# Kernel tuning notes

Measured on AMD Instinct MI355X. Metric: run time of the kernel, lower is better.

Reference implementation:

```python
import jax, jax.numpy as jnp
import numpy as np

N_HEAD = 12
D_HEAD = 64  # key_dim // n_head = 768 // 12


def sparsemax(z):
    # Martins & Astudillo (2016): projection of each row of z onto the simplex.
    K = z.shape[-1]
    z_sorted = -jnp.sort(-z, axis=-1)                      # descending sort
    cs = jnp.cumsum(z_sorted, axis=-1)
    r = jnp.arange(1, K + 1, dtype=z.dtype)
    support = (1.0 + r * z_sorted) > cs                    # support set indicator
    ksz = jnp.sum(support, axis=-1, keepdims=True)         # support size k(z)
    cs_k = jnp.take_along_axis(cs, ksz.astype(jnp.int32) - 1, axis=-1)
    tau = (cs_k - 1.0) / ksz.astype(z.dtype)               # threshold
    return jnp.maximum(z - tau, 0.0)


def setup_inputs() -> dict:
    key = jax.random.key(0)
    kq, kk, kv, kwq, kbq, kwk, kbk = jax.random.split(key, 7)
    B, L, D = 8, 1024, 768
    scale = 0.02
    return {
        "q": jax.random.normal(kq, (B, L, D), jnp.float32),
        "k": jax.random.normal(kk, (B, L, D), jnp.float32),
        "v": jax.random.normal(kv, (B, L, D), jnp.float32),
        "Wq": jax.random.normal(kwq, (D, D), jnp.float32) * scale,  # torch Linear weight [out,in]
        "bq": jax.random.normal(kbq, (D,), jnp.float32) * scale,
        "Wk": jax.random.normal(kwk, (D, D), jnp.float32) * scale,
        "bk": jax.random.normal(kbk, (D,), jnp.float32) * scale,
    }


def reference(q, k, v, Wq, bq, Wk, bk):
    B, Lq, _ = q.shape
    Lkv = k.shape[1]
    # project and split heads: [B, H, L, d_head]
    qh = (q @ Wq.T + bq).reshape(B, Lq, N_HEAD, D_HEAD).transpose(0, 2, 1, 3)
    kh = (k @ Wk.T + bk).reshape(B, Lkv, N_HEAD, D_HEAD).transpose(0, 2, 1, 3)
    inv_sqrt_d = jnp.asarray(1.0 / np.sqrt(D_HEAD), q.dtype)
    scores = jnp.einsum("bhqd,bhkd->bhqk", qh, kh) * inv_sqrt_d  # [B,H,Lq,Lkv]
    attn = sparsemax(scores)
    attn = attn.mean(axis=1)                                      # head-mean -> [B,Lq,Lkv]
    # eval mode: smooth_max is identity (training-only smoothing)
    output = jnp.einsum("bqk,bkd->bqd", attn, v)                  # [B,Lq,Dv]
    return output, attn
```

## Files before the change

kernel.cpp:

```cpp
#include <hip/hip_runtime.h>

#define BSZ 8
#define NH 12
#define LSEQ 1024
#define DMODEL 768
#define DHEAD 64
#define OUT_ELEMS 6291456
#define ATTN_ELEMS 8388608

typedef __attribute__((ext_vector_type(8))) short short8;
typedef __attribute__((ext_vector_type(4))) float f32x4;

__device__ __forceinline__ int   f2i(float x) { union { float f; int i; } c; c.f = x; return c.i; }
__device__ __forceinline__ float i2f(int x)   { union { int i; float f; } c; c.i = x; return c.f; }

__device__ __forceinline__ unsigned short f2bf(float x) {
    union { float f; unsigned u; } c; c.f = x;
    unsigned r = (c.u + 0x7FFF + ((c.u >> 16) & 1)) >> 16;
    return (unsigned short)r;
}
__device__ __forceinline__ float bf2f(unsigned short h) {
    union { float f; unsigned u; } c; c.u = ((unsigned)h) << 16;
    return c.f;
}
__device__ __forceinline__ void split2(float x, unsigned short& h, unsigned short& l) {
    h = f2bf(x);
    l = f2bf(x - bf2f(h));
}

template<int CTRL>
__device__ __forceinline__ float dppadd(float v) {
    return v + i2f(__builtin_amdgcn_update_dpp(0, f2i(v), CTRL, 0xF, 0xF, true));
}
template<int CTRL>
__device__ __forceinline__ float dppmax(float v) {
    return fmaxf(v, i2f(__builtin_amdgcn_update_dpp(f2i(v), f2i(v), CTRL, 0xF, 0xF, false)));
}

__device__ __forceinline__ void wsum2(float s[2]) {
#define WS(CTRL) _Pragma("unroll") for (int rr = 0; rr < 2; ++rr) { s[rr] = dppadd<CTRL>(s[rr]); }
    WS(0x111) WS(0x112) WS(0x114) WS(0x118) WS(0x142) WS(0x143)
#undef WS
#pragma unroll
    for (int rr = 0; rr < 2; ++rr) s[rr] = i2f(__builtin_amdgcn_readlane(f2i(s[rr]), 63));
}

__device__ __forceinline__ void wsummax2(float s[2], float m[2]) {
#define WS(CTRL) _Pragma("unroll") for (int rr = 0; rr < 2; ++rr) { s[rr] = dppadd<CTRL>(s[rr]); m[rr] = dppmax<CTRL>(m[rr]); }
    WS(0x111) WS(0x112) WS(0x114) WS(0x118) WS(0x142) WS(0x143)
#undef WS
#pragma unroll
    for (int rr = 0; rr < 2; ++rr) {
        s[rr] = i2f(__builtin_amdgcn_readlane(f2i(s[rr]), 63));
        m[rr] = i2f(__builtin_amdgcn_readlane(f2i(m[rr]), 63));
    }
}

__global__ __launch_bounds__(256) void proj_mfma(
    const float* __restrict__ qin, const float* __restrict__ kin,
    const float* __restrict__ Wq, const float* __restrict__ bq,
    const float* __restrict__ Wk, const float* __restrict__ bk,
    unsigned short* __restrict__ ws) {
    const float* A; const float* W; const float* bias;
    unsigned short* hi; unsigned short* lo;
    if (blockIdx.z == 0) { A = qin; W = Wq; bias = bq; hi = ws;                lo = ws + OUT_ELEMS; }
    else                 { A = kin; W = Wk; bias = bk; hi = ws + 2*OUT_ELEMS; lo = ws + 3*OUT_ELEMS; }

    __shared__ unsigned short Ah[128][32], Al[128][32];
    __shared__ unsigned short Bh[128][32], Bl[128][32];

    const int t    = threadIdx.x;
    const int lane = t & 63;
    const int w    = t >> 6;
    const int wr   = w >> 1, wc = w & 1;
    const int mrow = lane & 15, quad = lane >> 4;
    const int m0   = blockIdx.y * 128;
    const int n0   = blockIdx.x * 128;

    const int srow = t >> 3;
    const int scol = (t & 7) * 4;

    f32x4 acc[4][4];
#pragma unroll
    for (int i = 0; i < 4; ++i)
#pragma unroll
        for (int j = 0; j < 4; ++j) acc[i][j] = (f32x4){0.f, 0.f, 0.f, 0.f};

    for (int k0 = 0; k0 < DMODEL; k0 += 32) {
        float4 av[4], wv[4];
#pragma unroll
        for (int i = 0; i < 4; ++i) {
            av[i] = *(const float4*)&A[(size_t)(m0 + srow + i * 32) * DMODEL + k0 + scol];
            wv[i] = *(const float4*)&W[(size_t)(n0 + srow + i * 32) * DMODEL + k0 + scol];
        }
        __syncthreads();
#pragma unroll
        for (int i = 0; i < 4; ++i) {
            ushort4 h4, l4;
            split2(av[i].x, h4.x, l4.x); split2(av[i].y, h4.y, l4.y);
            split2(av[i].z, h4.z, l4.z); split2(av[i].w, h4.w, l4.w);
            *(ushort4*)&Ah[srow + i * 32][scol] = h4;
            *(ushort4*)&Al[srow + i * 32][scol] = l4;
            split2(wv[i].x, h4.x, l4.x); split2(wv[i].y, h4.y, l4.y);
            split2(wv[i].z, h4.z, l4.z); split2(wv[i].w, h4.w, l4.w);
            *(ushort4*)&Bh[srow + i * 32][scol] = h4;
            *(ushort4*)&Bl[srow + i * 32][scol] = l4;
        }
        __syncthreads();

        short8 ah[4], al[4], bh[4], bl[4];
#pragma unroll
        for (int i = 0; i < 4; ++i) {
            ah[i] = *(const short8*)&Ah[wr * 64 + i * 16 + mrow][quad * 8];
            al[i] = *(const short8*)&Al[wr * 64 + i * 16 + mrow][quad * 8];
            bh[i] = *(const short8*)&Bh[wc * 64 + i * 16 + mrow][quad * 8];
            bl[i] = *(const short8*)&Bl[wc * 64 + i * 16 + mrow][quad * 8];
        }
#pragma unroll
        for (int i = 0; i < 4; ++i)
#pragma unroll
            for (int j = 0; j < 4; ++j) {
                acc[i][j] = __builtin_amdgcn_mfma_f32_16x16x32_bf16(al[i], bh[j], acc[i][j], 0, 0, 0);
                acc[i][j] = __builtin_amdgcn_mfma_f32_16x16x32_bf16(ah[i], bl[j], acc[i][j], 0, 0, 0);
                acc[i][j] = __builtin_amdgcn_mfma_f32_16x16x32_bf16(ah[i], bh[j], acc[i][j], 0, 0, 0);
            }
    }

#pragma unroll
    for (int j = 0; j < 4; ++j) {
        const int ng = n0 + wc * 64 + j * 16 + mrow;
        const float bj = bias[ng];
        const int hh = ng >> 6, dd = ng & 63;
#pragma unroll
        for (int i = 0; i < 4; ++i) {
#pragma unroll
            for (int reg = 0; reg < 4; ++reg) {
                const int mg = m0 + wr * 64 + i * 16 + quad * 4 + reg;
                const float c = acc[i][j][reg] + bj;
                unsigned short ch, cl;
                split2(c, ch, cl);
                const size_t idx = (((size_t)(mg >> 10) * NH + hh) * LSEQ + (mg & 1023)) * DHEAD + dd;
                hi[idx] = ch;
                lo[idx] = cl;
            }
        }
    }
}

__global__ __launch_bounds__(512, 4) void attn_kernel(
    const unsigned short* __restrict__ ws, float* __restrict__ attn_out) {
    __shared__ float S[16 * 1024];

    const unsigned short* Qhi = ws;
    const unsigned short* Qlo = ws + OUT_ELEMS;
    const unsigned short* Khi = ws + 2 * OUT_ELEMS;
    const unsigned short* Klo = ws + 3 * OUT_ELEMS;

    const int t = threadIdx.x;
    const int lane = t & 63;
    const int w = t >> 6;
    const int b = blockIdx.y;
    const int q0 = blockIdx.x * 16;

    const int mrow = lane & 15;
    const int quad = lane >> 4;

    float macc[2][16];
#pragma unroll
    for (int rr = 0; rr < 2; ++rr)
#pragma unroll
        for (int j = 0; j < 16; ++j) macc[rr][j] = 0.f;

    for (int h = 0; h < NH; ++h) {
        const size_t hb = ((size_t)b * NH + h) * (LSEQ * DHEAD);

        const size_t aoff = hb + (size_t)(q0 + mrow) * DHEAD + quad * 8;
        short8 ah0 = *(const short8*)(Qhi + aoff);
        short8 ah1 = *(const short8*)(Qhi + aoff + 32);
        short8 al0 = *(const short8*)(Qlo + aoff);
        short8 al1 = *(const short8*)(Qlo + aoff + 32);

        __syncthreads();

#pragma unroll 2
        for (int nt = 0; nt < 8; ++nt) {
            const int n0 = w * 128 + nt * 16;
            const size_t boff = hb + (size_t)(n0 + mrow) * DHEAD + quad * 8;
            short8 bh0 = *(const short8*)(Khi + boff);
            short8 bh1 = *(const short8*)(Khi + boff + 32);
            short8 bl0 = *(const short8*)(Klo + boff);
            short8 bl1 = *(const short8*)(Klo + boff + 32);
            f32x4 d = {0.f, 0.f, 0.f, 0.f};
            d = __builtin_amdgcn_mfma_f32_16x16x32_bf16(al0, bh0, d, 0, 0, 0);
            d = __builtin_amdgcn_mfma_f32_16x16x32_bf16(ah0, bl0, d, 0, 0, 0);
            d = __builtin_amdgcn_mfma_f32_16x16x32_bf16(ah0, bh0, d, 0, 0, 0);
            d = __builtin_amdgcn_mfma_f32_16x16x32_bf16(al1, bh1, d, 0, 0, 0);
            d = __builtin_amdgcn_mfma_f32_16x16x32_bf16(ah1, bl1, d, 0, 0, 0);
            d = __builtin_amdgcn_mfma_f32_16x16x32_bf16(ah1, bh1, d, 0, 0, 0);
            const int swcol = (n0 + mrow) ^ (quad << 4);
#pragma unroll
            for (int reg = 0; reg < 4; ++reg)
                S[(quad * 4 + reg) * 1024 + swcol] = d[reg] * 0.125f;
        }
        __syncthreads();

        float z[2][16];
        float sv[2], mv[2];
#pragma unroll
        for (int rr = 0; rr < 2; ++rr) {
            const int r = w * 2 + rr;
            const int swz = (r >> 2) << 4;
#pragma unroll
            for (int c = 0; c < 4; ++c)
                *(f32x4*)&z[rr][c * 4] = *(const f32x4*)&S[r * 1024 + ((c * 256 + lane * 4) ^ swz)];
            float s0 = 0.f, s1 = 0.f, s2 = 0.f, s3 = 0.f;
            float m0 = z[rr][0], m1 = z[rr][1], m2 = z[rr][2], m3 = z[rr][3];
#pragma unroll
            for (int j = 0; j < 16; j += 4) {
                s0 += z[rr][j]; s1 += z[rr][j + 1]; s2 += z[rr][j + 2]; s3 += z[rr][j + 3];
            }
#pragma unroll
            for (int j = 4; j < 16; j += 4) {
                m0 = fmaxf(m0, z[rr][j]);     m1 = fmaxf(m1, z[rr][j + 1]);
                m2 = fmaxf(m2, z[rr][j + 2]); m3 = fmaxf(m3, z[rr][j + 3]);
            }
            sv[rr] = (s0 + s1) + (s2 + s3);
            mv[rr] = fmaxf(fmaxf(m0, m1), fmaxf(m2, m3));
        }
        wsummax2(sv, mv);

        float tau[2]; int prev[2]; bool done[2];
#pragma unroll
        for (int rr = 0; rr < 2; ++rr) {
            tau[rr] = fmaxf((sv[rr] - 1.0f) * (1.0f / 1024.0f), mv[rr] - 1.0f);
            prev[rr] = -1; done[rr] = false;
        }

        for (int it = 0; it < 64; ++it) {
            float sI[2]; int cI[2];
#pragma unroll
            for (int rr = 0; rr < 2; ++rr) {
                float a0 = 0.f, a1 = 0.f, a2 = 0.f, a3 = 0.f;
                int c = 0;
#pragma unroll
                for (int j = 0; j < 16; j += 4) {
                    bool g0 = z[rr][j]     > tau[rr];
                    bool g1 = z[rr][j + 1] > tau[rr];
                    bool g2 = z[rr][j + 2] > tau[rr];
                    bool g3 = z[rr][j + 3] > tau[rr];
                    c += __popcll(__ballot(g0)) + __popcll(__ballot(g1))
                       + __popcll(__ballot(g2)) + __popcll(__ballot(g3));
                    a0 += g0 ? z[rr][j]     : 0.f;
                    a1 += g1 ? z[rr][j + 1] : 0.f;
                    a2 += g2 ? z[rr][j + 2] : 0.f;
                    a3 += g3 ? z[rr][j + 3] : 0.f;
                }
                sI[rr] = (a0 + a1) + (a2 + a3);
                cI[rr] = c;
            }
            wsum2(sI);
            bool alldone = true;
#pragma unroll
            for (int rr = 0; rr < 2; ++rr) {
                if (!done[rr]) {
                    if (cI[rr] == prev[rr]) done[rr] = true;
                    else { tau[rr] = (sI[rr] - 1.0f) / (float)cI[rr]; prev[rr] = cI[rr]; }
                }
                alldone = alldone && done[rr];
            }
            if (alldone) break;
        }

#pragma unroll
        for (int rr = 0; rr < 2; ++rr)
#pragma unroll
            for (int j = 0; j < 16; ++j)
                macc[rr][j] += fmaxf(z[rr][j] - tau[rr], 0.f);
    }

    float* ao = attn_out + ((size_t)b * LSEQ + q0) * LSEQ;
#pragma unroll
    for (int rr = 0; rr < 2; ++rr) {
        const int r = w * 2 + rr;
#pragma unroll
        for (int c = 0; c < 4; ++c) {
            f32x4 o;
#pragma unroll
            for (int j = 0; j < 4; ++j) o[j] = macc[rr][c * 4 + j] * (1.0f / 12.0f);
            *(f32x4*)&ao[(size_t)r * LSEQ + c * 256 + lane * 4] = o;
        }
    }
}

__global__ __launch_bounds__(256) void out_mfma(
    const float* __restrict__ attn, const float* __restrict__ v,
    float* __restrict__ out) {
    const int b = blockIdx.z;
    const float* Ab = attn + (size_t)b * LSEQ * LSEQ;
    const float* Vb = v    + (size_t)b * LSEQ * DMODEL;
    float* Cb       = out  + (size_t)b * LSEQ * DMODEL;

    __shared__ unsigned short Ah[128][32], Al[128][32];
    __shared__ unsigned short Bh[128][36], Bl[128][36];

    const int t    = threadIdx.x;
    const int lane = t & 63;
    const int w    = t >> 6;
    const int wr   = w >> 1, wc = w & 1;
    const int mrow = lane & 15, quad = lane >> 4;
    const int m0   = blockIdx.y * 128;
    const int n0   = blockIdx.x * 128;

    const int srow = t >> 3;
    const int scol = (t & 7) * 4;
    const int bn   = t & 127;
    const int bk0  = (t >> 7) * 16;

    f32x4 acc[4][4];
#pragma unroll
    for (int i = 0; i < 4; ++i)
#pragma unroll
        for (int j = 0; j < 4; ++j) acc[i][j] = (f32x4){0.f, 0.f, 0.f, 0.f};

    for (int k0 = 0; k0 < LSEQ; k0 += 32) {
        float4 av[4];
#pragma unroll
        for (int i = 0; i < 4; ++i)
            av[i] = *(const float4*)&Ab[(size_t)(m0 + srow + i * 32) * LSEQ + k0 + scol];
        float bv[16];
#pragma unroll
        for (int i = 0; i < 16; ++i)
            bv[i] = Vb[(size_t)(k0 + bk0 + i) * DMODEL + n0 + bn];

        __syncthreads();
#pragma unroll
        for (int i = 0; i < 4; ++i) {
            ushort4 h4, l4;
            split2(av[i].x, h4.x, l4.x); split2(av[i].y, h4.y, l4.y);
            split2(av[i].z, h4.z, l4.z); split2(av[i].w, h4.w, l4.w);
            *(ushort4*)&Ah[srow + i * 32][scol] = h4;
            *(ushort4*)&Al[srow + i * 32][scol] = l4;
        }
#pragma unroll
        for (int g = 0; g < 4; ++g) {
            ushort4 h4, l4;
            split2(bv[g * 4 + 0], h4.x, l4.x); split2(bv[g * 4 + 1], h4.y, l4.y);
            split2(bv[g * 4 + 2], h4.z, l4.z); split2(bv[g * 4 + 3], h4.w, l4.w);
            *(ushort4*)&Bh[bn][bk0 + g * 4] = h4;
            *(ushort4*)&Bl[bn][bk0 + g * 4] = l4;
        }
        __syncthreads();

        short8 ah[4], al[4], bh[4], bl[4];
#pragma unroll
        for (int i = 0; i < 4; ++i) {
            ah[i] = *(const short8*)&Ah[wr * 64 + i * 16 + mrow][quad * 8];
            al[i] = *(const short8*)&Al[wr * 64 + i * 16 + mrow][quad * 8];
        }
#pragma unroll
        for (int j = 0; j < 4; ++j) {
            const unsigned short* ph = &Bh[wc * 64 + j * 16 + mrow][quad * 8];
            const unsigned short* pl = &Bl[wc * 64 + j * 16 + mrow][quad * 8];
            uint2 h0 = *(const uint2*)ph;
            uint2 h1 = *(const uint2*)(ph + 4);
            uint2 l0 = *(const uint2*)pl;
            uint2 l1 = *(const uint2*)(pl + 4);
            union { uint u[4]; short8 s; } ch, cl;
            ch.u[0] = h0.x; ch.u[1] = h0.y; ch.u[2] = h1.x; ch.u[3] = h1.y;
            cl.u[0] = l0.x; cl.u[1] = l0.y; cl.u[2] = l1.x; cl.u[3] = l1.y;
            bh[j] = ch.s; bl[j] = cl.s;
        }
#pragma unroll
        for (int i = 0; i < 4; ++i)
#pragma unroll
            for (int j = 0; j < 4; ++j) {
                acc[i][j] = __builtin_amdgcn_mfma_f32_16x16x32_bf16(al[i], bh[j], acc[i][j], 0, 0, 0);
                acc[i][j] = __builtin_amdgcn_mfma_f32_16x16x32_bf16(ah[i], bl[j], acc[i][j], 0, 0, 0);
                acc[i][j] = __builtin_amdgcn_mfma_f32_16x16x32_bf16(ah[i], bh[j], acc[i][j], 0, 0, 0);
            }
    }

#pragma unroll
    for (int i = 0; i < 4; ++i)
#pragma unroll
        for (int j = 0; j < 4; ++j)
#pragma unroll
            for (int reg = 0; reg < 4; ++reg) {
                const int mg = m0 + wr * 64 + i * 16 + quad * 4 + reg;
                const int ng = n0 + wc * 64 + j * 16 + mrow;
                Cb[(size_t)mg * DMODEL + ng] = acc[i][j][reg];
            }
}

extern "C" void kernel_launch(void* const* d_in, const int* in_sizes, int n_in,
                              void* d_out, int out_size, void* d_ws, size_t ws_size,
                              hipStream_t stream) {
    const float* q  = (const float*)d_in[0];
    const float* k  = (const float*)d_in[1];
    const float* v  = (const float*)d_in[2];
    const float* Wq = (const float*)d_in[3];
    const float* bq = (const float*)d_in[4];
    const float* Wk = (const float*)d_in[5];
    const float* bk = (const float*)d_in[6];

    float* out  = (float*)d_out;
    float* attn = out + OUT_ELEMS;
    unsigned short* ws = (unsigned short*)d_ws;

    hipLaunchKernelGGL(proj_mfma, dim3(6, 64, 2), dim3(256), 0, stream,
                       q, k, Wq, bq, Wk, bk, ws);
    hipLaunchKernelGGL(attn_kernel, dim3(64, 8), dim3(512), 0, stream,
                       ws, attn);
    hipLaunchKernelGGL(out_mfma, dim3(6, 8, 8), dim3(256), 0, stream,
                       attn, v, out);
}
```

Measured before the change: 511.7 us.

## Software-pipeline K loads, prefetch next-head Q, and remap blocks for cache locality

```diff
diff --git a/kernel.cpp b/kernel.cpp
--- a/kernel.cpp
+++ b/kernel.cpp
@@ -159,8 +159,10 @@
     const int t = threadIdx.x;
     const int lane = t & 63;
     const int w = t >> 6;
-    const int b = blockIdx.y;
-    const int q0 = blockIdx.x * 16;
+    const int idlin = blockIdx.x + 64 * blockIdx.y;
+    const int b  = idlin & 7;
+    const int q0 = (idlin >> 3) * 16;
+    const int hoff = ((idlin >> 3) & 1) * 6;
 
     const int mrow = lane & 15;
     const int quad = lane >> 4;
@@ -171,37 +173,56 @@
 #pragma unroll
         for (int j = 0; j < 16; ++j) macc[rr][j] = 0.f;
 
-    for (int h = 0; h < NH; ++h) {
-        const size_t hb = ((size_t)b * NH + h) * (LSEQ * DHEAD);
-
-        const size_t aoff = hb + (size_t)(q0 + mrow) * DHEAD + quad * 8;
-        short8 ah0 = *(const short8*)(Qhi + aoff);
-        short8 ah1 = *(const short8*)(Qhi + aoff + 32);
-        short8 al0 = *(const short8*)(Qlo + aoff);
-        short8 al1 = *(const short8*)(Qlo + aoff + 32);
-
-        __syncthreads();
-
-#pragma unroll 2
-        for (int nt = 0; nt < 8; ++nt) {
-            const int n0 = w * 128 + nt * 16;
-            const size_t boff = hb + (size_t)(n0 + mrow) * DHEAD + quad * 8;
-            short8 bh0 = *(const short8*)(Khi + boff);
-            short8 bh1 = *(const short8*)(Khi + boff + 32);
-            short8 bl0 = *(const short8*)(Klo + boff);
-            short8 bl1 = *(const short8*)(Klo + boff + 32);
-            f32x4 d = {0.f, 0.f, 0.f, 0.f};
-            d = __builtin_amdgcn_mfma_f32_16x16x32_bf16(al0, bh0, d, 0, 0, 0);
-            d = __builtin_amdgcn_mfma_f32_16x16x32_bf16(ah0, bl0, d, 0, 0, 0);
-            d = __builtin_amdgcn_mfma_f32_16x16x32_bf16(ah0, bh0, d, 0, 0, 0);
-            d = __builtin_amdgcn_mfma_f32_16x16x32_bf16(al1, bh1, d, 0, 0, 0);
-            d = __builtin_amdgcn_mfma_f32_16x16x32_bf16(ah1, bl1, d, 0, 0, 0);
-            d = __builtin_amdgcn_mfma_f32_16x16x32_bf16(ah1, bh1, d, 0, 0, 0);
-            const int swcol = (n0 + mrow) ^ (quad << 4);
-#pragma unroll
-            for (int reg = 0; reg < 4; ++reg)
-                S[(quad * 4 + reg) * 1024 + swcol] = d[reg] * 0.125f;
-        }
+    size_t hb;
+    short8 qh0, qh1, ql0, ql1;
+    short8 kah0, kah1, kal0, kal1;
+    short8 kbh0, kbh1, kbl0, kbl1;
+    short8 kch0, kch1, kcl0, kcl1;
+
+#define QLOAD() do { \
+    const size_t aoff_ = hb + (size_t)(q0 + mrow) * DHEAD + quad * 8; \
+    qh0 = *(const short8*)(Qhi + aoff_); \
+    qh1 = *(const short8*)(Qhi + aoff_ + 32); \
+    ql0 = *(const short8*)(Qlo + aoff_); \
+    ql1 = *(const short8*)(Qlo + aoff_ + 32); \
+} while (0)
+
+#define KLOAD(P, nt) do { \
+    const size_t boff_ = hb + (size_t)(w * 128 + (nt) * 16 + mrow) * DHEAD + quad * 8; \
+    P##h0 = *(const short8*)(Khi + boff_); \
+    P##h1 = *(const short8*)(Khi + boff_ + 32); \
+    P##l0 = *(const short8*)(Klo + boff_); \
+    P##l1 = *(const short8*)(Klo + boff_ + 32); \
+} while (0)
+
+#define KMFMA(P, nt) do { \
+    f32x4 d_ = (f32x4){0.f, 0.f, 0.f, 0.f}; \
+    d_ = __builtin_amdgcn_mfma_f32_16x16x32_bf16(ql0, P##h0, d_, 0, 0, 0); \
+    d_ = __builtin_amdgcn_mfma_f32_16x16x32_bf16(qh0, P##l0, d_, 0, 0, 0); \
+    d_ = __builtin_amdgcn_mfma_f32_16x16x32_bf16(qh0, P##h0, d_, 0, 0, 0); \
+    d_ = __builtin_amdgcn_mfma_f32_16x16x32_bf16(ql1, P##h1, d_, 0, 0, 0); \
+    d_ = __builtin_amdgcn_mfma_f32_16x16x32_bf16(qh1, P##l1, d_, 0, 0, 0); \
+    d_ = __builtin_amdgcn_mfma_f32_16x16x32_bf16(qh1, P##h1, d_, 0, 0, 0); \
+    const int swcol_ = (w * 128 + (nt) * 16 + mrow) ^ (quad << 4); \
+    _Pragma("unroll") for (int reg = 0; reg < 4; ++reg) \
+        S[(quad * 4 + reg) * 1024 + swcol_] = d_[reg] * 0.125f; \
+} while (0)
+
+    hb = ((size_t)b * NH + hoff) * (LSEQ * DHEAD);
+    QLOAD();
+
+#pragma unroll 1
+    for (int i = 0; i < NH; ++i) {
+        __syncthreads();
+
+        KLOAD(ka, 0); KLOAD(kb, 1);
+        KLOAD(kc, 2); KMFMA(ka, 0);
+        KLOAD(ka, 3); KMFMA(kb, 1);
+        KLOAD(kb, 4); KMFMA(kc, 2);
+        KLOAD(kc, 5); KMFMA(ka, 3);
+        KLOAD(ka, 6); KMFMA(kb, 4);
+        KLOAD(kb, 7); KMFMA(kc, 5);
+        KMFMA(ka, 6); KMFMA(kb, 7);
         __syncthreads();
 
         float z[2][16];
@@ -213,6 +234,16 @@
 #pragma unroll
             for (int c = 0; c < 4; ++c)
                 *(f32x4*)&z[rr][c * 4] = *(const f32x4*)&S[r * 1024 + ((c * 256 + lane * 4) ^ swz)];
+        }
+
+        if (i + 1 < NH) {
+            int hn = i + 1 + hoff; if (hn >= NH) hn -= NH;
+            hb = ((size_t)b * NH + hn) * (LSEQ * DHEAD);
+            QLOAD();
+        }
+
+#pragma unroll
+        for (int rr = 0; rr < 2; ++rr) {
             float s0 = 0.f, s1 = 0.f, s2 = 0.f, s3 = 0.f;
             float m0 = z[rr][0], m1 = z[rr][1], m2 = z[rr][2], m3 = z[rr][3];
 #pragma unroll
@@ -290,6 +321,9 @@
             *(f32x4*)&ao[(size_t)r * LSEQ + c * 256 + lane * 4] = o;
         }
     }
+#undef QLOAD
+#undef KLOAD
+#undef KMFMA
 }
 
 __global__ __launch_bounds__(256) void out_mfma(
```

New measurement: 512.3 us. Within noise of the previous version (+0.1%).

## Use one row per wave with a statistical sparsemax threshold guess

Applied to the files above, without the earlier changes.

```diff
diff --git a/kernel.cpp b/kernel.cpp
--- a/kernel.cpp
+++ b/kernel.cpp
@@ -45,15 +45,13 @@
     for (int rr = 0; rr < 2; ++rr) s[rr] = i2f(__builtin_amdgcn_readlane(f2i(s[rr]), 63));
 }
 
-__device__ __forceinline__ void wsummax2(float s[2], float m[2]) {
-#define WS(CTRL) _Pragma("unroll") for (int rr = 0; rr < 2; ++rr) { s[rr] = dppadd<CTRL>(s[rr]); m[rr] = dppmax<CTRL>(m[rr]); }
+__device__ __forceinline__ void wred3(float& s, float& q, float& m) {
+#define WS(CTRL) { s = dppadd<CTRL>(s); q = dppadd<CTRL>(q); m = dppmax<CTRL>(m); }
     WS(0x111) WS(0x112) WS(0x114) WS(0x118) WS(0x142) WS(0x143)
 #undef WS
-#pragma unroll
-    for (int rr = 0; rr < 2; ++rr) {
-        s[rr] = i2f(__builtin_amdgcn_readlane(f2i(s[rr]), 63));
-        m[rr] = i2f(__builtin_amdgcn_readlane(f2i(m[rr]), 63));
-    }
+    s = i2f(__builtin_amdgcn_readlane(f2i(s), 63));
+    q = i2f(__builtin_amdgcn_readlane(f2i(q), 63));
+    m = i2f(__builtin_amdgcn_readlane(f2i(m), 63));
 }
 
 __global__ __launch_bounds__(256) void proj_mfma(
@@ -147,7 +145,7 @@
     }
 }
 
-__global__ __launch_bounds__(512, 4) void attn_kernel(
+__global__ __launch_bounds__(1024, 8) void attn_kernel(
     const unsigned short* __restrict__ ws, float* __restrict__ attn_out) {
     __shared__ float S[16 * 1024];
 
@@ -159,136 +157,141 @@
     const int t = threadIdx.x;
     const int lane = t & 63;
     const int w = t >> 6;
-    const int b = blockIdx.y;
-    const int q0 = blockIdx.x * 16;
+    const int idlin = blockIdx.x;
+    const int b  = idlin & 7;
+    const int q0 = (idlin >> 3) * 16;
 
     const int mrow = lane & 15;
     const int quad = lane >> 4;
 
-    float macc[2][16];
-#pragma unroll
-    for (int rr = 0; rr < 2; ++rr)
-#pragma unroll
-        for (int j = 0; j < 16; ++j) macc[rr][j] = 0.f;
-
+    float macc[16];
+#pragma unroll
+    for (int j = 0; j < 16; ++j) macc[j] = 0.f;
+
+#pragma unroll 1
     for (int h = 0; h < NH; ++h) {
         const size_t hb = ((size_t)b * NH + h) * (LSEQ * DHEAD);
 
-        const size_t aoff = hb + (size_t)(q0 + mrow) * DHEAD + quad * 8;
-        short8 ah0 = *(const short8*)(Qhi + aoff);
-        short8 ah1 = *(const short8*)(Qhi + aoff + 32);
-        short8 al0 = *(const short8*)(Qlo + aoff);
-        short8 al1 = *(const short8*)(Qlo + aoff + 32);
-
-        __syncthreads();
-
-#pragma unroll 2
-        for (int nt = 0; nt < 8; ++nt) {
-            const int n0 = w * 128 + nt * 16;
-            const size_t boff = hb + (size_t)(n0 + mrow) * DHEAD + quad * 8;
-            short8 bh0 = *(const short8*)(Khi + boff);
-            short8 bh1 = *(const short8*)(Khi + boff + 32);
-            short8 bl0 = *(const short8*)(Klo + boff);
-            short8 bl1 = *(const short8*)(Klo + boff + 32);
-            f32x4 d = {0.f, 0.f, 0.f, 0.f};
-            d = __builtin_amdgcn_mfma_f32_16x16x32_bf16(al0, bh0, d, 0, 0, 0);
-            d = __builtin_amdgcn_mfma_f32_16x16x32_bf16(ah0, bl0, d, 0, 0, 0);
-            d = __builtin_amdgcn_mfma_f32_16x16x32_bf16(ah0, bh0, d, 0, 0, 0);
-            d = __builtin_amdgcn_mfma_f32_16x16x32_bf16(al1, bh1, d, 0, 0, 0);
-            d = __builtin_amdgcn_mfma_f32_16x16x32_bf16(ah1, bl1, d, 0, 0, 0);
-            d = __builtin_amdgcn_mfma_f32_16x16x32_bf16(ah1, bh1, d, 0, 0, 0);
-            const int swcol = (n0 + mrow) ^ (quad << 4);
-#pragma unroll
-            for (int reg = 0; reg < 4; ++reg)
-                S[(quad * 4 + reg) * 1024 + swcol] = d[reg] * 0.125f;
-        }
-        __syncthreads();
-
-        float z[2][16];
-        float sv[2], mv[2];
-#pragma unroll
-        for (int rr = 0; rr < 2; ++rr) {
-            const int r = w * 2 + rr;
-            const int swz = (r >> 2) << 4;
+        {
+            const size_t aoff = hb + (size_t)(q0 + mrow) * DHEAD + quad * 8;
+            short8 qh0 = *(const short8*)(Qhi + aoff);
+            short8 qh1 = *(const short8*)(Qhi + aoff + 32);
+            short8 ql0 = *(const short8*)(Qlo + aoff);
+            short8 ql1 = *(const short8*)(Qlo + aoff + 32);
+#pragma unroll
+            for (int nt = 0; nt < 4; ++nt) {
+                const int n0 = w * 64 + nt * 16;
+                const size_t boff = hb + (size_t)(n0 + mrow) * DHEAD + quad * 8;
+                short8 kh0 = *(const short8*)(Khi + boff);
+                short8 kh1 = *(const short8*)(Khi + boff + 32);
+                short8 kl0 = *(const short8*)(Klo + boff);
+                short8 kl1 = *(const short8*)(Klo + boff + 32);
+                f32x4 d = (f32x4){0.f, 0.f, 0.f, 0.f};
+                d = __builtin_amdgcn_mfma_f32_16x16x32_bf16(ql0, kh0, d, 0, 0, 0);
+                d = __builtin_amdgcn_mfma_f32_16x16x32_bf16(qh0, kl0, d, 0, 0, 0);
+                d = __builtin_amdgcn_mfma_f32_16x16x32_bf16(qh0, kh0, d, 0, 0, 0);
+                d = __builtin_amdgcn_mfma_f32_16x16x32_bf16(ql1, kh1, d, 0, 0, 0);
+                d = __builtin_amdgcn_mfma_f32_16x16x32_bf16(qh1, kl1, d, 0, 0, 0);
+                d = __builtin_amdgcn_mfma_f32_16x16x32_bf16(qh1, kh1, d, 0, 0, 0);
+                const int swcol = (n0 + mrow) ^ (quad << 4);
+#pragma unroll
+                for (int reg = 0; reg < 4; ++reg)
+                    S[(quad * 4 + reg) * 1024 + swcol] = d[reg] * 0.125f;
+            }
+        }
+        __syncthreads();
+
+        float z[16];
+        {
+            const int swz = ((w >> 2) & 3) << 4;
 #pragma unroll
             for (int c = 0; c < 4; ++c)
-                *(f32x4*)&z[rr][c * 4] = *(const f32x4*)&S[r * 1024 + ((c * 256 + lane * 4) ^ swz)];
+                *(f32x4*)&z[c * 4] = *(const f32x4*)&S[w * 1024 + ((c * 256 + lane * 4) ^ swz)];
+        }
+        __syncthreads();
+
+        float sv, qv, mv;
+        {
             float s0 = 0.f, s1 = 0.f, s2 = 0.f, s3 = 0.f;
-            float m0 = z[rr][0], m1 = z[rr][1], m2 = z[rr][2], m3 = z[rr][3];
+            float p0 = 0.f, p1 = 0.f, p2 = 0.f, p3 = 0.f;
+            float m0 = z[0], m1 = z[1], m2 = z[2], m3 = z[3];
 #pragma unroll
             for (int j = 0; j < 16; j += 4) {
-                s0 += z[rr][j]; s1 += z[rr][j + 1]; s2 += z[rr][j + 2]; s3 += z[rr][j + 3];
+                s0 += z[j]; s1 += z[j + 1]; s2 += z[j + 2]; s3 += z[j + 3];
+                p0 = fmaf(z[j],     z[j],     p0);
+                p1 = fmaf(z[j + 1], z[j + 1], p1);
+                p2 = fmaf(z[j + 2], z[j + 2], p2);
+                p3 = fmaf(z[j + 3], z[j + 3], p3);
             }
 #pragma unroll
             for (int j = 4; j < 16; j += 4) {
-                m0 = fmaxf(m0, z[rr][j]);     m1 = fmaxf(m1, z[rr][j + 1]);
-                m2 = fmaxf(m2, z[rr][j + 2]); m3 = fmaxf(m3, z[rr][j + 3]);
-            }
-            sv[rr] = (s0 + s1) + (s2 + s3);
-            mv[rr] = fmaxf(fmaxf(m0, m1), fmaxf(m2, m3));
-        }
-        wsummax2(sv, mv);
-
-        float tau[2]; int prev[2]; bool done[2];
-#pragma unroll
-        for (int rr = 0; rr < 2; ++rr) {
-            tau[rr] = fmaxf((sv[rr] - 1.0f) * (1.0f / 1024.0f), mv[rr] - 1.0f);
-            prev[rr] = -1; done[rr] = false;
-        }
-
-        for (int it = 0; it < 64; ++it) {
-            float sI[2]; int cI[2];
-#pragma unroll
-            for (int rr = 0; rr < 2; ++rr) {
-                float a0 = 0.f, a1 = 0.f, a2 = 0.f, a3 = 0.f;
-                int c = 0;
-#pragma unroll
-                for (int j = 0; j < 16; j += 4) {
-                    bool g0 = z[rr][j]     > tau[rr];
-                    bool g1 = z[rr][j + 1] > tau[rr];
-                    bool g2 = z[rr][j + 2] > tau[rr];
-                    bool g3 = z[rr][j + 3] > tau[rr];
-                    c += __popcll(__ballot(g0)) + __popcll(__ballot(g1))
-                       + __popcll(__ballot(g2)) + __popcll(__ballot(g3));
-                    a0 += g0 ? z[rr][j]     : 0.f;
-                    a1 += g1 ? z[rr][j + 1] : 0.f;
-                    a2 += g2 ? z[rr][j + 2] : 0.f;
-                    a3 += g3 ? z[rr][j + 3] : 0.f;
-                }
-                sI[rr] = (a0 + a1) + (a2 + a3);
-                cI[rr] = c;
-            }
-            wsum2(sI);
-            bool alldone = true;
-#pragma unroll
-            for (int rr = 0; rr < 2; ++rr) {
-                if (!done[rr]) {
-                    if (cI[rr] == prev[rr]) done[rr] = true;
-                    else { tau[rr] = (sI[rr] - 1.0f) / (float)cI[rr]; prev[rr] = cI[rr]; }
-                }
-                alldone = alldone && done[rr];
-            }
-            if (alldone) break;
-        }
-
-#pragma unroll
-        for (int rr = 0; rr < 2; ++rr)
-#pragma unroll
-            for (int j = 0; j < 16; ++j)
-                macc[rr][j] += fmaxf(z[rr][j] - tau[rr], 0.f);
+                m0 = fmaxf(m0, z[j]);     m1 = fmaxf(m1, z[j + 1]);
+                m2 = fmaxf(m2, z[j + 2]); m3 = fmaxf(m3, z[j + 3]);
+            }
+            sv = (s0 + s1) + (s2 + s3);
+            qv = (p0 + p1) + (p2 + p3);
+            mv = fmaxf(fmaxf(m0, m1), fmaxf(m2, m3));
+        }
+        wred3(sv, qv, mv);
+
+        const float t0s = fmaxf((sv - 1.0f) * (1.0f / 1024.0f), mv - 1.0f);
+        float tau;
+        {
+            const float mu  = sv * (1.0f / 1024.0f);
+            const float var = fmaxf(qv * (1.0f / 1024.0f) - mu * mu, 1e-12f);
+            const float sg  = sqrtf(var);
+            const float a   = 2.7196f + 0.33333f * __logf(sg);
+            const float tg  = mu + (a - 0.25f) * sg;
+            tau = fminf(fmaxf(tg, t0s), mv - 1e-3f);
+        }
+
+#define SP_PASS(SC) do { \
+        float a0 = 0.f, a1 = 0.f, a2 = 0.f, a3 = 0.f; \
+        float n0 = 0.f, n1 = 0.f, n2 = 0.f, n3 = 0.f; \
+        _Pragma("unroll") for (int j = 0; j < 16; j += 4) { \
+            bool g0 = z[j]     > tau; \
+            bool g1 = z[j + 1] > tau; \
+            bool g2 = z[j + 2] > tau; \
+            bool g3 = z[j + 3] > tau; \
+            a0 += g0 ? z[j]     : 0.f;  n0 += g0 ? 1.f : 0.f; \
+            a1 += g1 ? z[j + 1] : 0.f;  n1 += g1 ? 1.f : 0.f; \
+            a2 += g2 ? z[j + 2] : 0.f;  n2 += g2 ? 1.f : 0.f; \
+            a3 += g3 ? z[j + 3] : 0.f;  n3 += g3 ? 1.f : 0.f; \
+        } \
+        SC[0] = (a0 + a1) + (a2 + a3); \
+        SC[1] = (n0 + n1) + (n2 + n3); \
+        wsum2(SC); \
+} while (0)
+
+        float prev;
+        {
+            float sc[2];
+            SP_PASS(sc);
+            const float tn = (sc[0] - 1.0f) / sc[1];
+            if (tn >= tau) { tau = tn; prev = sc[1]; }
+            else           { tau = t0s; prev = -1.f; }
+        }
+        for (int it = 0; it < 63; ++it) {
+            float sc[2];
+            SP_PASS(sc);
+            if (sc[1] == prev) break;
+            tau = (sc[0] - 1.0f) / sc[1];
+            prev = sc[1];
+        }
+#undef SP_PASS
+
+#pragma unroll
+        for (int j = 0; j < 16; ++j)
+            macc[j] += fmaxf(z[j] - tau, 0.f);
     }
 
     float* ao = attn_out + ((size_t)b * LSEQ + q0) * LSEQ;
 #pragma unroll
-    for (int rr = 0; rr < 2; ++rr) {
-        const int r = w * 2 + rr;
-#pragma unroll
-        for (int c = 0; c < 4; ++c) {
-            f32x4 o;
-#pragma unroll
-            for (int j = 0; j < 4; ++j) o[j] = macc[rr][c * 4 + j] * (1.0f / 12.0f);
-            *(f32x4*)&ao[(size_t)r * LSEQ + c * 256 + lane * 4] = o;
-        }
+    for (int c = 0; c < 4; ++c) {
+        f32x4 o;
+#pragma unroll
+        for (int j = 0; j < 4; ++j) o[j] = macc[c * 4 + j] * (1.0f / 12.0f);
+        *(f32x4*)&ao[(size_t)w * LSEQ + c * 256 + lane * 4] = o;
     }
 }
 
@@ -409,7 +412,7 @@
 
     hipLaunchKernelGGL(proj_mfma, dim3(6, 64, 2), dim3(256), 0, stream,
                        q, k, Wq, bq, Wk, bk, ws);
-    hipLaunchKernelGGL(attn_kernel, dim3(64, 8), dim3(512), 0, stream,
+    hipLaunchKernelGGL(attn_kernel, dim3(512), dim3(1024), 0, stream,
                        ws, attn);
     hipLaunchKernelGGL(out_mfma, dim3(6, 8, 8), dim3(256), 0, stream,
                        attn, v, out);
```

Result: no change. 518.3 us (+1.3%).
